# Kernel optimization log

Measured on AMD Instinct MI355X. Metric: run time of the kernel, lower is better.

## Reference

```python
import jax, jax.numpy as jnp
import numpy as np

BN_EPS = 1e-5
L2_EPS = 1e-12


def setup_inputs() -> dict:
    key = jax.random.key(0)
    ks = jax.random.split(key, 4)
    B, C, H, W = 16, 384, 56, 56
    x = jax.random.normal(ks[0], (B, C, H, W), dtype=jnp.float32)
    w_qkv = jax.random.normal(ks[1], (3 * C, C), dtype=jnp.float32) * (1.0 / np.sqrt(C))
    b_qkv = jnp.zeros((3 * C,), dtype=jnp.float32)
    w_proj = jax.random.normal(ks[2], (C, C), dtype=jnp.float32) * (1.0 / np.sqrt(C))
    b_proj = jnp.zeros((C,), dtype=jnp.float32)
    bn_gamma = jnp.ones((C,), dtype=jnp.float32)
    bn_beta = jnp.zeros((C,), dtype=jnp.float32)
    bn_mean = jnp.zeros((C,), dtype=jnp.float32)
    bn_var = jnp.ones((C,), dtype=jnp.float32)
    temperature = jnp.ones((1,), dtype=jnp.float32)
    return {"x": x, "w_qkv": w_qkv, "b_qkv": b_qkv, "w_proj": w_proj,
            "b_proj": b_proj, "bn_gamma": bn_gamma, "bn_beta": bn_beta,
            "bn_mean": bn_mean, "bn_var": bn_var, "temperature": temperature}


def _l2norm_lastdim(t):
    # F.normalize(t, dim=-1): divide by max(||t||_2, eps)
    n = jnp.sqrt(jnp.sum(t * t, axis=-1, keepdims=True))
    return t / jnp.maximum(n, L2_EPS)


def reference(x, w_qkv, b_qkv, w_proj, b_proj, bn_gamma, bn_beta, bn_mean, bn_var, temperature):
    B, C, H, W = x.shape
    N = H * W
    # BatchNorm2d (eval mode, running stats)
    scale = bn_gamma / jnp.sqrt(bn_var + BN_EPS)          # [C]
    shift = bn_beta - bn_mean * scale                     # [C]
    xn = x * scale[None, :, None, None] + shift[None, :, None, None]
    # 1x1 conv qkv: C -> 3C, operate on flattened spatial [B, C, N]
    xn_f = xn.reshape(B, C, N)
    qkv = jnp.einsum('oc,bcn->bon', w_qkv, xn_f) + b_qkv[None, :, None]  # [B,3C,N]
    q, k, v = qkv[:, :C], qkv[:, C:2 * C], qkv[:, 2 * C:]
    q = _l2norm_lastdim(q)                                # [B,C,N]
    k = _l2norm_lastdim(k)
    # channel-transposed attention: [B,C,C]
    logits = jnp.einsum('bcn,bdn->bcd', q, k) * temperature[0]
    attn = jax.nn.softmax(logits, axis=-1)
    fused = jnp.einsum('bcd,bdn->bcn', attn, v)           # [B,C,N]
    # 1x1 proj conv + residual
    out = jnp.einsum('oc,bcn->bon', w_proj, fused) + b_proj[None, :, None]
    return x + out.reshape(B, C, H, W)
```

## Files before the change

kernel.cpp:

```cpp
#include <hip/hip_runtime.h>

#define BATCH 16
#define CCH   384
#define NSP   3136
#define NSPP  3200

typedef unsigned short u16;
typedef float  f32x4  __attribute__((ext_vector_type(4)));
typedef __bf16 bf16x8 __attribute__((ext_vector_type(8)));

__device__ __forceinline__ float bf2f(u16 u) {
  union { unsigned int i; float f; } v; v.i = ((unsigned int)u) << 16; return v.f;
}
__device__ __forceinline__ u16 f2bf(float f) {
  union { float f; unsigned int i; } v; v.f = f;
  unsigned int i = v.i;
  return (u16)((i + 0x7fffu + ((i >> 16) & 1u)) >> 16);
}
__device__ __forceinline__ float rdf(const void* p, long i, bool bf) {
  return bf ? bf2f(((const u16*)p)[i]) : ((const float*)p)[i];
}

__device__ __forceinline__ void gload_lds16(const u16* g, u16* l) {
  __builtin_amdgcn_global_load_lds(
      (const __attribute__((address_space(1))) void*)g,
      (__attribute__((address_space(3))) void*)l, 16, 0, 0);
}

__global__ void transpose_kernel(const void* __restrict__ x, u16* __restrict__ xt,
                                 u16* __restrict__ xbf, const u16* __restrict__ probe) {
  const bool bf = (probe[0] == 0x3F80u);
  __shared__ float Ls[32 * 65];
  const int t = threadIdx.x;
  const int n0 = blockIdx.x * 64, c0 = blockIdx.y * 32, b = blockIdx.z;
  if (n0 >= NSP) {
    const int n_l = t >> 2, c8 = (t & 3) * 8;
    uint4 zq = make_uint4(0, 0, 0, 0);
    *(uint4*)(xt + ((long)b * NSPP + n0 + n_l) * CCH + c0 + c8) = zq;
    return;
  }
  {
    const int c_l = t >> 3, n8 = (t & 7) * 8;
    const long src = ((long)b * CCH + c0 + c_l) * NSP + n0 + n8;
    float v[8];
    if (bf) {
      union { uint4 q; u16 e[8]; } u; u.q = *(const uint4*)((const u16*)x + src);
      #pragma unroll
      for (int i = 0; i < 8; i++) v[i] = bf2f(u.e[i]);
    } else {
      float4 a = *(const float4*)((const float*)x + src);
      float4 c = *(const float4*)((const float*)x + src + 4);
      v[0]=a.x; v[1]=a.y; v[2]=a.z; v[3]=a.w; v[4]=c.x; v[5]=c.y; v[6]=c.z; v[7]=c.w;
    }
    union { uint4 q; u16 e[8]; } ob;
    #pragma unroll
    for (int i = 0; i < 8; i++) { ob.e[i] = f2bf(v[i]); Ls[c_l * 65 + n8 + i] = v[i]; }
    *(uint4*)(xbf + src) = ob.q;
  }
  __syncthreads();
  {
    const int n_l = t >> 2, c8 = (t & 3) * 8;
    union { uint4 q; u16 e[8]; } o;
    #pragma unroll
    for (int i = 0; i < 8; i++) o.e[i] = f2bf(Ls[(c8 + i) * 65 + n_l]);
    *(uint4*)(xt + ((long)b * NSPP + n0 + n_l) * CCH + c0 + c8) = o.q;
  }
}

__global__ void prep_kernel(const void* __restrict__ w_qkv, const void* __restrict__ b_qkv,
                            const void* __restrict__ gamma, const void* __restrict__ beta,
                            const void* __restrict__ mean,  const void* __restrict__ var,
                            const void* __restrict__ b_proj, const void* __restrict__ w_proj,
                            u16* __restrict__ w_eff, float* __restrict__ b_eff,
                            float* __restrict__ bproj_f,
                            unsigned* __restrict__ w2qk, unsigned* __restrict__ wp2,
                            u16* __restrict__ wvT, float* __restrict__ szero,
                            const u16* __restrict__ probe) {
  const bool bf = (probe[0] == 0x3F80u);
  __shared__ float s_scale[CCH], s_shift[CCH];
  const int tid = threadIdx.x;
  const int o = blockIdx.x;
  if (o < 72) {
    szero[o * 256 + tid] = 0.f;
    szero[o * 256 + 128 + tid] = 0.f;
  }
  for (int c = tid; c < CCH; c += 128) {
    float g = rdf(gamma, c, bf), bt = rdf(beta, c, bf);
    float mn = rdf(mean, c, bf), vr = rdf(var, c, bf);
    float sc = g * rsqrtf(vr + 1e-5f);
    s_scale[c] = sc; s_shift[c] = bt - mn * sc;
  }
  __syncthreads();
  float part = 0.f;
  for (int c = tid; c < CCH; c += 128) {
    float w = rdf(w_qkv, (long)o * CCH + c, bf);
    u16 wv = f2bf(w * s_scale[c]);
    w_eff[(long)o * CCH + c] = wv;
    if (o < 768) w2qk[(long)o * CCH + c] = (unsigned)wv | ((unsigned)wv << 16);
    else         wvT[(long)c * CCH + (o - 768)] = wv;
    part += w * s_shift[c];
  }
  for (int off = 32; off > 0; off >>= 1) part += __shfl_down(part, off, 64);
  __shared__ float s_part[2];
  if ((tid & 63) == 0) s_part[tid >> 6] = part;
  __syncthreads();
  if (tid == 0) b_eff[o] = rdf(b_qkv, o, bf) + s_part[0] + s_part[1];
  if (o < CCH) {
    for (int c = tid; c < CCH; c += 128) {
      u16 pv = f2bf(rdf(w_proj, (long)o * CCH + c, bf));
      wp2[(long)o * CCH + c] = (unsigned)pv | ((unsigned)pv << 16);
    }
  }
  if (o == 0) {
    for (int c = tid; c < CCH; c += 128) bproj_f[c] = rdf(b_proj, c, bf);
  }
}

template<int BM, int BN, int WGM, int WGN, int OUTM, bool BIASM, bool RES,
         int NCHK, bool EPIL, bool SUMX, bool SYMM>
__launch_bounds__(256)
__global__ void gemm_nt(const u16* __restrict__ A, const u16* __restrict__ B,
                        void* __restrict__ Cv,
                        const float* __restrict__ biasm,
                        const void* __restrict__ resv,
                        int K, int lda, int ldb, int ldc,
                        long sA, long sB, long sC, long sRes,
                        int zb, int nLim, int ks, int sBM,
                        float* __restrict__ qns, const u16* __restrict__ epW,
                        float* __restrict__ sxp,
                        const u16* __restrict__ probe) {
  constexpr int WM = BM / WGM, WN = BN / WGN;
  constexpr int FM = WM / 16,  FN = WN / 16;
  constexpr int NA = BM / 32,  NB = BN / 32;
  constexpr bool BOUNCE = (OUTM == 1 || OUTM == 2) && (BM == BN) && (WGM == 2) && (WGN == 2);
  const bool f32io = (probe[0] != 0x3F80u);
  __shared__ __align__(16) u16 As[BM * 64];
  __shared__ __align__(16) u16 Bs[BN * 64];
  const int tid = threadIdx.x, wave = tid >> 6, lane = tid & 63;
  const int quad = lane >> 4, l16 = lane & 15;
  const int wm = wave / WGN, wn = wave % WGN;
  int z = blockIdx.z, kc = 0;
  if (ks > 1) { kc = z % ks; z /= ks; }
  A += z * sA; B += z * sB;
  const long cOff = (long)(zb + z) * sC;
  const long rOff = (long)(zb + z) * sRes;

  const int gx = gridDim.x;
  const int tot = gx * gridDim.y;
  const int wg = blockIdx.y * gx + blockIdx.x;
  const int qq = tot >> 3, rr = tot & 7;
  const int xcd = wg & 7, idx = wg >> 3;
  const int nid = (xcd < rr ? xcd * (qq + 1) : rr * (qq + 1) + (xcd - rr) * qq) + idx;
  const int m0 = (nid % gx) * BM, n0 = (nid / gx) * BN;
  if (SYMM && n0 > m0) return;

  const int kLen = K / ks, kBeg = kc * kLen;

  const u16* ag[NA];
  const u16* bg[NB];
  #pragma unroll
  for (int p = 0; p < NA; p++) {
    int u = tid + p * 256, r = u >> 3, k8 = u & 7;
    ag[p] = A + (long)(m0 + r) * lda + kBeg + ((k8 ^ (r & 7)) << 3);
  }
  #pragma unroll
  for (int p = 0; p < NB; p++) {
    int u = tid + p * 256, r = u >> 3, k8 = u & 7;
    bg[p] = B + (long)(n0 + r) * ldb + kBeg + ((k8 ^ (r & 7)) << 3);
  }

  f32x4 acc[FM][FN] = {};
  float rs[FM] = {};

  const int nt = kLen >> 6;
  for (int t = 0; t < nt; t++) {
    #pragma unroll
    for (int p = 0; p < NA; p++) { gload_lds16(ag[p], &As[(p * 256 + wave * 64) * 8]); ag[p] += 64; }
    #pragma unroll
    for (int p = 0; p < NB; p++) { gload_lds16(bg[p], &Bs[(p * 256 + wave * 64) * 8]); bg[p] += 64; }
    __syncthreads();

    #pragma unroll
    for (int tt = 0; tt < 2; tt++) {
      bf16x8 af[FM], bfr[FN];
      #pragma unroll
      for (int f = 0; f < FM; f++) {
        int r = wm * WM + f * 16 + l16;
        af[f] = *(const bf16x8*)&As[r * 64 + (((tt * 4 + quad) ^ (l16 & 7)) << 3)];
      }
      #pragma unroll
      for (int g = 0; g < FN; g++) {
        int r = wn * WN + g * 16 + l16;
        bfr[g] = *(const bf16x8*)&Bs[r * 64 + (((tt * 4 + quad) ^ (l16 & 7)) << 3)];
      }
      if (SUMX) {
        if (n0 == 0 && wn == 0) {
          #pragma unroll
          for (int f = 0; f < FM; f++)
            #pragma unroll
            for (int j = 0; j < 8; j++) rs[f] += (float)af[f][j];
        }
      }
      #pragma unroll
      for (int f = 0; f < FM; f++)
        #pragma unroll
        for (int g = 0; g < FN; g++)
          acc[f][g] = __builtin_amdgcn_mfma_f32_16x16x32_bf16(af[f], bfr[g], acc[f][g], 0, 0, 0);
    }
    __syncthreads();
  }

  if (SUMX) {
    if (n0 == 0 && wn == 0) {
      #pragma unroll
      for (int f = 0; f < FM; f++) {
        float r = rs[f];
        r += __shfl_xor(r, 16, 64);
        r += __shfl_xor(r, 32, 64);
        if (quad == 0) atomicAdd(sxp + (long)z * CCH + m0 + wm * WM + f * 16 + l16, r);
      }
    }
  }

  if (BOUNCE) {
    float* Lb = (float*)As;
    const long cBase = cOff + ((OUTM == 1 && ks > 1) ? (long)kc * sRes : 0L);
    #pragma unroll
    for (int f = 0; f < FM; f++) {
      #pragma unroll
      for (int g = 0; g < FN; g++)
        #pragma unroll
        for (int reg = 0; reg < 4; reg++) {
          float v = acc[f][g][reg];
          if (BIASM) v += biasm[(long)(zb + z) * sBM + m0 + wm * WM + f * 16 + quad * 4 + reg];
          Lb[(wm * 16 + quad * 4 + reg) * BN + wn * WN + g * 16 + l16] = v;
        }
      __syncthreads();
      {
        const int tr = tid >> 3;
        const int cb = (tid & 7) * (BN / 8);
        const int mm = m0 + (tr >> 4) * WM + f * 16 + (tr & 15);
        const long rowBase = (long)mm * ldc;
        #pragma unroll
        for (int j = 0; j < BN / 32; j++) {
          const int nn = n0 + cb + j * 4;
          const bool live = (NCHK != 2) || (nn < nLim);
          if (live) {
            float4 v = *(const float4*)&Lb[tr * BN + cb + j * 4];
            if (RES) {
              if (f32io) {
                float4 r = *(const float4*)&((const float*)resv)[rOff + rowBase + nn];
                v.x += r.x; v.y += r.y; v.z += r.z; v.w += r.w;
              } else {
                const u16* rp = (const u16*)resv + rOff + rowBase + nn;
                v.x += bf2f(rp[0]); v.y += bf2f(rp[1]); v.z += bf2f(rp[2]); v.w += bf2f(rp[3]);
              }
            }
            if (OUTM == 1 || f32io) {
              *(float4*)&((float*)Cv)[cBase + rowBase + nn] = v;
            } else {
              ushort4 o4 = { f2bf(v.x), f2bf(v.y), f2bf(v.z), f2bf(v.w) };
              *(ushort4*)((u16*)Cv + cOff + rowBase + nn) = o4;
            }
          }
        }
      }
      __syncthreads();
    }
  } else {
    #pragma unroll
    for (int f = 0; f < FM; f++) {
      #pragma unroll
      for (int reg = 0; reg < 4; reg++) {
        const int mm = m0 + wm * WM + f * 16 + quad * 4 + reg;
        float s2 = 0.f;
        #pragma unroll
        for (int g = 0; g < FN; g++) {
          int nn = n0 + wn * WN + g * 16 + l16;
          float v = acc[f][g][reg];
          if (BIASM) v += biasm[(long)(zb + z) * sBM + mm];
          long off = (long)mm * ldc + nn;
          bool live = true;
          if (NCHK == 2) live = (nn < nLim);
          if (NCHK == 3) live = (mm < nLim);
          if (RES && live) {
            long ro = rOff + off;
            v += f32io ? ((const float*)resv)[ro] : bf2f(((const u16*)resv)[ro]);
          }
          if (EPIL) s2 += v * bf2f(epW[(long)mm * CCH + nn]);
          if (OUTM == 1) {
            ((float*)Cv)[cOff + off + (long)kc * sRes] = v;
          } else if (OUTM == 2) {
            if (live) {
              if (f32io) ((float*)Cv)[cOff + off] = v;
              else       ((u16*)Cv)[cOff + off]   = f2bf(v);
            }
          } else if (OUTM == 4) {
            if (live) {
              u16 hi = f2bf(v);
              u16 lo = f2bf(v - bf2f(hi));
              ((unsigned*)Cv)[cOff + off] = (unsigned)hi | ((unsigned)lo << 16);
            }
          } else {
            if (live) ((u16*)Cv)[cOff + off] = f2bf(v);
          }
        }
        if (EPIL) {
          s2 += __shfl_xor(s2, 1, 16);
          s2 += __shfl_xor(s2, 2, 16);
          s2 += __shfl_xor(s2, 4, 16);
          s2 += __shfl_xor(s2, 8, 16);
          if (l16 == 0) atomicAdd(qns + (long)(zb + z) * 768 + mm, s2);
        }
      }
    }
  }
}

__global__ void gred_ugemv_kernel(const float* __restrict__ Gp, unsigned* __restrict__ Gs,
                                  const u16* __restrict__ w_eff, const float* __restrict__ sx,
                                  float* __restrict__ u, int kspl) {
  const int b = blockIdx.y, bx = blockIdx.x, tid = threadIdx.x;
  if (bx < 576) {
    const int idx = bx * 256 + tid;
    const int r = idx / CCH, c = idx % CCH;
    const long e = ((r >> 7) >= (c >> 7)) ? ((long)r * CCH + c) : ((long)c * CCH + r);
    const long base = (long)b * kspl * (CCH * CCH);
    float s = 0.f;
    for (int k = 0; k < kspl; k++) s += Gp[base + (long)k * (CCH * CCH) + e];
    u16 hi = f2bf(s);
    u16 lo = f2bf(s - bf2f(hi));
    Gs[(long)b * (CCH * CCH) + idx] = (unsigned)hi | ((unsigned)lo << 16);
  } else {
    const int m = (bx - 576) * 4 + (tid >> 6), l = tid & 63;
    float s = 0.f;
    for (int k = l; k < CCH; k += 64) s += bf2f(w_eff[(long)m * CCH + k]) * sx[b * CCH + k];
    for (int off = 32; off > 0; off >>= 1) s += __shfl_down(s, off, 64);
    if (l == 0) u[b * 768 + m] = s;
  }
}

__global__ void cgemv_kernel(const unsigned* __restrict__ wp2, const float* __restrict__ av,
                             const float* __restrict__ bproj, float* __restrict__ cvec) {
  const int o = blockIdx.x, b = blockIdx.y, l = threadIdx.x;
  float s = 0.f;
  for (int c = l; c < CCH; c += 64)
    s += bf2f((u16)(wp2[(long)o * CCH + c] & 0xffffu)) * av[b * CCH + c];
  for (int off = 32; off > 0; off >>= 1) s += __shfl_down(s, off, 64);
  if (l == 0) cvec[b * CCH + o] = s + bproj[o];
}

__global__ void softmax_kernel(const float* __restrict__ Lg, const float* __restrict__ qn2,
                               const float* __restrict__ u, const float* __restrict__ beff,
                               const void* __restrict__ temp,
                               u16* __restrict__ attn, float* __restrict__ av,
                               const u16* __restrict__ probe) {
  const bool bfm = (probe[0] == 0x3F80u);
  const int c = blockIdx.x, b = blockIdx.y, tid = threadIdx.x;
  const float* row = Lg + ((long)b * CCH + c) * CCH;
  const float beq = beff[c], uq = u[b * 768 + c];
  const float qn = qn2[b * 768 + c] + 2.f * beq * uq + 3136.f * beq * beq;
  const float rq = 1.f / fmaxf(sqrtf(fmaxf(qn, 0.f)), 1e-12f);
  const float T = rdf(temp, 0, bfm);
  float v[3]; float mx = -1e30f;
  #pragma unroll
  for (int j = 0; j < 3; j++) {
    int d = tid + j * 128;
    float bek = beff[384 + d], uk = u[b * 768 + 384 + d];
    float kn = qn2[b * 768 + 384 + d] + 2.f * bek * uk + 3136.f * bek * bek;
    float rd = 1.f / fmaxf(sqrtf(fmaxf(kn, 0.f)), 1e-12f);
    float lg = row[d] + uq * bek + beq * uk + 3136.f * beq * bek;
    v[j] = lg * rq * rd * T;
    mx = fmaxf(mx, v[j]);
  }
  for (int off = 32; off > 0; off >>= 1) mx = fmaxf(mx, __shfl_down(mx, off, 64));
  __shared__ float sm[2];
  if ((tid & 63) == 0) sm[tid >> 6] = mx;
  __syncthreads();
  mx = fmaxf(sm[0], sm[1]);
  float s = 0.f;
  #pragma unroll
  for (int j = 0; j < 3; j++) { v[j] = __expf(v[j] - mx); s += v[j]; }
  for (int off = 32; off > 0; off >>= 1) s += __shfl_down(s, off, 64);
  __shared__ float ss[2];
  if ((tid & 63) == 0) ss[tid >> 6] = s;
  __syncthreads();
  s = ss[0] + ss[1];
  const float inv = 1.f / s;
  float avp = 0.f;
  u16* arow = attn + ((long)b * CCH + c) * CCH;
  #pragma unroll
  for (int j = 0; j < 3; j++) {
    float p = v[j] * inv;
    arow[tid + j * 128] = f2bf(p);
    avp += p * beff[768 + tid + j * 128];
  }
  for (int off = 32; off > 0; off >>= 1) avp += __shfl_down(avp, off, 64);
  __shared__ float sa[2];
  if ((tid & 63) == 0) sa[tid >> 6] = avp;
  __syncthreads();
  if (tid == 0) av[b * CCH + c] = sa[0] + sa[1];
}

extern "C" void kernel_launch(void* const* d_in, const int* in_sizes, int n_in,
                              void* d_out, int out_size, void* d_ws, size_t ws_size,
                              hipStream_t stream) {
  const void* x      = d_in[0];
  const void* w_qkv  = d_in[1];
  const void* b_qkv  = d_in[2];
  const void* w_proj = d_in[3];
  const void* b_proj = d_in[4];
  const void* gamma  = d_in[5];
  const void* beta   = d_in[6];
  const void* mean   = d_in[7];
  const void* var    = d_in[8];
  const void* temp   = d_in[9];
  const u16* probe = (const u16*)gamma;

  const size_t SZ_XT   = (size_t)BATCH * NSPP * CCH * 2;
  const size_t SZ_XBF  = (size_t)BATCH * CCH * NSP * 2;
  const size_t SZ_WEFF = (size_t)1152 * CCH * 2;
  const size_t SZ_W2QK = (size_t)768 * CCH * 4;
  const size_t SZ_WP2  = (size_t)CCH * CCH * 4;
  const size_t SZ_WVT  = (size_t)CCH * CCH * 2;
  const size_t SZ_BEFF = (size_t)1152 * 4;
  const size_t SZ_BPRJ = (size_t)CCH * 4;
  const size_t SZ_U    = (size_t)BATCH * 768 * 4;
  const size_t SZ_AV   = (size_t)BATCH * CCH * 4;
  const size_t SZ_CV   = (size_t)BATCH * CCH * 4;
  const size_t SZ_MM   = (size_t)BATCH * CCH * CCH;
  const size_t FIXED = SZ_XT + SZ_XBF + SZ_WEFF + SZ_W2QK + SZ_WP2 + SZ_WVT +
                       SZ_BEFF + SZ_BPRJ + (size_t)BATCH * (CCH + 768) * 4 +
                       SZ_U + SZ_AV + SZ_CV +
                       SZ_MM * 4  + SZ_MM * 4  + SZ_MM * 4  +
                       SZ_MM * 2  + SZ_MM * 4  + SZ_MM * 2 ;
  int kspl = 7;
  if (ws_size < FIXED + (size_t)BATCH * 7 * CCH * CCH * 4) kspl = 1;

  char* ws = (char*)d_ws;
  u16*      xt    = (u16*)ws;      ws += SZ_XT;
  u16*      xbf   = (u16*)ws;      ws += SZ_XBF;
  u16*      w_eff = (u16*)ws;      ws += SZ_WEFF;
  unsigned* w2qk  = (unsigned*)ws; ws += SZ_W2QK;
  unsigned* wp2   = (unsigned*)ws; ws += SZ_WP2;
  u16*      wvT   = (u16*)ws;      ws += SZ_WVT;
  float*    b_eff = (float*)ws;    ws += SZ_BEFF;
  float*    bproj = (float*)ws;    ws += SZ_BPRJ;
  float*    sx    = (float*)ws;    ws += (size_t)BATCH * CCH * 4;
  float*    qn2   = (float*)ws;    ws += (size_t)BATCH * 768 * 4;
  float*    u     = (float*)ws;    ws += SZ_U;
  float*    av    = (float*)ws;    ws += SZ_AV;
  float*    cvec  = (float*)ws;    ws += SZ_CV;
  unsigned* Gs    = (unsigned*)ws; ws += SZ_MM * 4;
  unsigned* Ts    = (unsigned*)ws; ws += SZ_MM * 4;
  float*    Lg    = (float*)ws;    ws += SZ_MM * 4;
  u16*      attn  = (u16*)ws;      ws += SZ_MM * 2;
  unsigned* RTs   = (unsigned*)ws; ws += SZ_MM * 4;
  u16*      Mb    = (u16*)ws;      ws += SZ_MM * 2;
  float*    Gp    = (float*)ws;

  const long sXB = (long)CCH * NSP;
  const long sMM = (long)CCH * CCH;
  const long sM2 = (long)CCH * 768;

  transpose_kernel<<<dim3(NSPP / 64, CCH / 32, BATCH), dim3(256), 0, stream>>>(
      x, xt, xbf, probe);
  prep_kernel<<<dim3(1152), dim3(128), 0, stream>>>(
      w_qkv, b_qkv, gamma, beta, mean, var, b_proj, w_proj,
      w_eff, b_eff, bproj, w2qk, wp2, wvT, sx, probe);

  gemm_nt<128, 128, 2, 2, 1, false, false, 0, false, true, true>
      <<<dim3(3, 3, BATCH * kspl), dim3(256), 0, stream>>>(
      xbf, xbf, Gp, nullptr, nullptr,
      NSP, NSP, NSP, CCH, sXB, sXB, (long)kspl * sMM, sMM,
      0, 0, kspl, 0, nullptr, nullptr, sx, probe);

  gred_ugemv_kernel<<<dim3(768, BATCH), dim3(256), 0, stream>>>(
      Gp, Gs, w_eff, sx, u, kspl);

  gemm_nt<96, 96, 2, 2, 4, false, false, 3, true, false, false>
      <<<dim3(8, 4, BATCH), dim3(256), 0, stream>>>(
      (const u16*)w2qk, (const u16*)Gs, Ts, nullptr, nullptr,
      768, 768, 768, CCH, 0L, sM2, sMM, 0L,
      0, CCH, 1, 0, qn2, w_eff, nullptr, probe);

  gemm_nt<96, 96, 2, 2, 1, false, false, 0, false, false, false>
      <<<dim3(4, 4, BATCH), dim3(256), 0, stream>>>(
      (const u16*)Ts, (const u16*)w2qk + (long)384 * 768, Lg, nullptr, nullptr,
      768, 768, 768, CCH, sM2, 0L, sMM, 0L,
      0, 0, 1, 0, nullptr, nullptr, nullptr, probe);

  softmax_kernel<<<dim3(CCH, BATCH), dim3(128), 0, stream>>>(
      Lg, qn2, u, b_eff, temp, attn, av, probe);

  gemm_nt<96, 96, 2, 2, 4, false, false, 0, false, false, false>
      <<<dim3(4, 4, BATCH), dim3(256), 0, stream>>>(
      wvT, attn, RTs, nullptr, nullptr,
      CCH, CCH, CCH, CCH, 0L, sMM, sMM, 0L,
      0, 0, 1, 0, nullptr, nullptr, nullptr, probe);

  cgemv_kernel<<<dim3(CCH, BATCH), dim3(64), 0, stream>>>(wp2, av, bproj, cvec);

  gemm_nt<96, 96, 2, 2, 0, false, false, 0, false, false, false>
      <<<dim3(4, 4, BATCH), dim3(256), 0, stream>>>(
      (const u16*)wp2, (const u16*)RTs, Mb, nullptr, nullptr,
      768, 768, 768, CCH, 0L, sM2, sMM, 0L,
      0, 0, 1, 0, nullptr, nullptr, nullptr, probe);

  gemm_nt<128, 128, 2, 2, 2, true, true, 2, false, false, false>
      <<<dim3(3, 25, BATCH), dim3(256), 0, stream>>>(
      Mb, xt, d_out, cvec, x,
      CCH, CCH, CCH, NSP, sMM, (long)NSPP * CCH, (long)CCH * NSP, (long)CCH * NSP,
      0, NSP, 1, CCH, nullptr, nullptr, nullptr, probe);
}
```

Baseline: 378.0 us.

## Drop split-K Gram GEMM and write packed output directly with mirror pass

The X·Xᵀ Gram GEMM no longer splits K into 7 chunks that write fp32 partials to a large workspace buffer. Each block now runs the full K=3136 loop and writes the packed hi/lo bf16 result straight into Gs. A lighter kernel then copies the computed lower-triangle tiles into the missing upper-triangle tiles, alongside the existing u GEMV. This removes the write and reduction of the per-batch partial Gram buffers, at the cost of far fewer blocks (96 active) each running a long serial K loop. The LDS bounce buffer is also padded by 4 floats per row to reduce bank conflicts.

```diff
diff --git a/kernel.cpp b/kernel.cpp
--- a/kernel.cpp
+++ b/kernel.cpp
@@ -125,22 +125,27 @@
                         const void* __restrict__ resv,
                         int K, int lda, int ldb, int ldc,
                         long sA, long sB, long sC, long sRes,
-                        int zb, int nLim, int ks, int sBM,
+                        int zb, int nLim, int sBM,
                         float* __restrict__ qns, const u16* __restrict__ epW,
                         float* __restrict__ sxp,
                         const u16* __restrict__ probe) {
   constexpr int WM = BM / WGM, WN = BN / WGN;
   constexpr int FM = WM / 16,  FN = WN / 16;
   constexpr int NA = BM / 32,  NB = BN / 32;
-  constexpr bool BOUNCE = (OUTM == 1 || OUTM == 2) && (BM == BN) && (WGM == 2) && (WGN == 2);
+  constexpr bool BOUNCE = (OUTM == 1 || OUTM == 2) && (BM == BN) && (WGN == 2);
+  constexpr int RPF = WGM * 16;
+  constexpr int LBS = BN + 4;
+  constexpr int SM_STAGE  = (BM + BN) * 128;
+  constexpr int SM_BOUNCE = BOUNCE ? RPF * LBS * 4 : 0;
+  constexpr int SM_BYTES  = SM_STAGE > SM_BOUNCE ? SM_STAGE : SM_BOUNCE;
+  __shared__ __align__(16) char smem[SM_BYTES];
+  u16* As = (u16*)smem;
+  u16* Bs = (u16*)(smem + BM * 128);
   const bool f32io = (probe[0] != 0x3F80u);
-  __shared__ __align__(16) u16 As[BM * 64];
-  __shared__ __align__(16) u16 Bs[BN * 64];
   const int tid = threadIdx.x, wave = tid >> 6, lane = tid & 63;
   const int quad = lane >> 4, l16 = lane & 15;
   const int wm = wave / WGN, wn = wave % WGN;
-  int z = blockIdx.z, kc = 0;
-  if (ks > 1) { kc = z % ks; z /= ks; }
+  const int z = blockIdx.z;
   A += z * sA; B += z * sB;
   const long cOff = (long)(zb + z) * sC;
   const long rOff = (long)(zb + z) * sRes;
@@ -154,25 +159,23 @@
   const int m0 = (nid % gx) * BM, n0 = (nid / gx) * BN;
   if (SYMM && n0 > m0) return;
 
-  const int kLen = K / ks, kBeg = kc * kLen;
-
   const u16* ag[NA];
   const u16* bg[NB];
   #pragma unroll
   for (int p = 0; p < NA; p++) {
     int u = tid + p * 256, r = u >> 3, k8 = u & 7;
-    ag[p] = A + (long)(m0 + r) * lda + kBeg + ((k8 ^ (r & 7)) << 3);
+    ag[p] = A + (long)(m0 + r) * lda + ((k8 ^ (r & 7)) << 3);
   }
   #pragma unroll
   for (int p = 0; p < NB; p++) {
     int u = tid + p * 256, r = u >> 3, k8 = u & 7;
-    bg[p] = B + (long)(n0 + r) * ldb + kBeg + ((k8 ^ (r & 7)) << 3);
+    bg[p] = B + (long)(n0 + r) * ldb + ((k8 ^ (r & 7)) << 3);
   }
 
   f32x4 acc[FM][FN] = {};
   float rs[FM] = {};
 
-  const int nt = kLen >> 6;
+  const int nt = K >> 6;
   for (int t = 0; t < nt; t++) {
     #pragma unroll
     for (int p = 0; p < NA; p++) { gload_lds16(ag[p], &As[(p * 256 + wave * 64) * 8]); ag[p] += 64; }
@@ -223,8 +226,7 @@
   }
 
   if (BOUNCE) {
-    float* Lb = (float*)As;
-    const long cBase = cOff + ((OUTM == 1 && ks > 1) ? (long)kc * sRes : 0L);
+    float* Lb = (float*)smem;
     #pragma unroll
     for (int f = 0; f < FM; f++) {
       #pragma unroll
@@ -233,7 +235,7 @@
         for (int reg = 0; reg < 4; reg++) {
           float v = acc[f][g][reg];
           if (BIASM) v += biasm[(long)(zb + z) * sBM + m0 + wm * WM + f * 16 + quad * 4 + reg];
-          Lb[(wm * 16 + quad * 4 + reg) * BN + wn * WN + g * 16 + l16] = v;
+          Lb[(wm * 16 + quad * 4 + reg) * LBS + wn * WN + g * 16 + l16] = v;
         }
       __syncthreads();
       {
@@ -246,7 +248,7 @@
           const int nn = n0 + cb + j * 4;
           const bool live = (NCHK != 2) || (nn < nLim);
           if (live) {
-            float4 v = *(const float4*)&Lb[tr * BN + cb + j * 4];
+            float4 v = *(const float4*)&Lb[tr * LBS + cb + j * 4];
             if (RES) {
               if (f32io) {
                 float4 r = *(const float4*)&((const float*)resv)[rOff + rowBase + nn];
@@ -257,7 +259,7 @@
               }
             }
             if (OUTM == 1 || f32io) {
-              *(float4*)&((float*)Cv)[cBase + rowBase + nn] = v;
+              *(float4*)&((float*)Cv)[cOff + rowBase + nn] = v;
             } else {
               ushort4 o4 = { f2bf(v.x), f2bf(v.y), f2bf(v.z), f2bf(v.w) };
               *(ushort4*)((u16*)Cv + cOff + rowBase + nn) = o4;
@@ -289,7 +291,7 @@
           }
           if (EPIL) s2 += v * bf2f(epW[(long)mm * CCH + nn]);
           if (OUTM == 1) {
-            ((float*)Cv)[cOff + off + (long)kc * sRes] = v;
+            ((float*)Cv)[cOff + off] = v;
           } else if (OUTM == 2) {
             if (live) {
               if (f32io) ((float*)Cv)[cOff + off] = v;
@@ -317,22 +319,21 @@
   }
 }
 
-__global__ void gred_ugemv_kernel(const float* __restrict__ Gp, unsigned* __restrict__ Gs,
-                                  const u16* __restrict__ w_eff, const float* __restrict__ sx,
-                                  float* __restrict__ u, int kspl) {
+__global__ void mirror_ugemv_kernel(unsigned* __restrict__ Gs,
+                                    const u16* __restrict__ w_eff,
+                                    const float* __restrict__ sx,
+                                    float* __restrict__ u) {
   const int b = blockIdx.y, bx = blockIdx.x, tid = threadIdx.x;
-  if (bx < 576) {
-    const int idx = bx * 256 + tid;
-    const int r = idx / CCH, c = idx % CCH;
-    const long e = ((r >> 7) >= (c >> 7)) ? ((long)r * CCH + c) : ((long)c * CCH + r);
-    const long base = (long)b * kspl * (CCH * CCH);
-    float s = 0.f;
-    for (int k = 0; k < kspl; k++) s += Gp[base + (long)k * (CCH * CCH) + e];
-    u16 hi = f2bf(s);
-    u16 lo = f2bf(s - bf2f(hi));
-    Gs[(long)b * (CCH * CCH) + idx] = (unsigned)hi | ((unsigned)lo << 16);
+  if (bx < 192) {
+    const int q = bx >> 6;
+    const int e = (bx & 63) * 256 + tid;
+    const int r = e >> 7, c = e & 127;
+    const int r0 = (q == 2) ? 128 : 0;
+    const int c0 = (q == 0) ? 128 : 256;
+    const long base = (long)b * (CCH * CCH);
+    Gs[base + (long)(r0 + r) * CCH + (c0 + c)] = Gs[base + (long)(c0 + c) * CCH + (r0 + r)];
   } else {
-    const int m = (bx - 576) * 4 + (tid >> 6), l = tid & 63;
+    const int m = (bx - 192) * 4 + (tid >> 6), l = tid & 63;
     float s = 0.f;
     for (int k = l; k < CCH; k += 64) s += bf2f(w_eff[(long)m * CCH + k]) * sx[b * CCH + k];
     for (int off = 32; off > 0; off >>= 1) s += __shfl_down(s, off, 64);
@@ -429,13 +430,6 @@
   const size_t SZ_AV   = (size_t)BATCH * CCH * 4;
   const size_t SZ_CV   = (size_t)BATCH * CCH * 4;
   const size_t SZ_MM   = (size_t)BATCH * CCH * CCH;
-  const size_t FIXED = SZ_XT + SZ_XBF + SZ_WEFF + SZ_W2QK + SZ_WP2 + SZ_WVT +
-                       SZ_BEFF + SZ_BPRJ + (size_t)BATCH * (CCH + 768) * 4 +
-                       SZ_U + SZ_AV + SZ_CV +
-                       SZ_MM * 4  + SZ_MM * 4  + SZ_MM * 4  +
-                       SZ_MM * 2  + SZ_MM * 4  + SZ_MM * 2 ;
-  int kspl = 7;
-  if (ws_size < FIXED + (size_t)BATCH * 7 * CCH * CCH * 4) kspl = 1;
 
   char* ws = (char*)d_ws;
   u16*      xt    = (u16*)ws;      ws += SZ_XT;
@@ -457,7 +451,6 @@
   u16*      attn  = (u16*)ws;      ws += SZ_MM * 2;
   unsigned* RTs   = (unsigned*)ws; ws += SZ_MM * 4;
   u16*      Mb    = (u16*)ws;      ws += SZ_MM * 2;
-  float*    Gp    = (float*)ws;
 
   const long sXB = (long)CCH * NSP;
   const long sMM = (long)CCH * CCH;
@@ -469,26 +462,26 @@
       w_qkv, b_qkv, gamma, beta, mean, var, b_proj, w_proj,
       w_eff, b_eff, bproj, w2qk, wp2, wvT, sx, probe);
 
-  gemm_nt<128, 128, 2, 2, 1, false, false, 0, false, true, true>
-      <<<dim3(3, 3, BATCH * kspl), dim3(256), 0, stream>>>(
-      xbf, xbf, Gp, nullptr, nullptr,
-      NSP, NSP, NSP, CCH, sXB, sXB, (long)kspl * sMM, sMM,
-      0, 0, kspl, 0, nullptr, nullptr, sx, probe);
-
-  gred_ugemv_kernel<<<dim3(768, BATCH), dim3(256), 0, stream>>>(
-      Gp, Gs, w_eff, sx, u, kspl);
+  gemm_nt<128, 128, 2, 2, 4, false, false, 0, false, true, true>
+      <<<dim3(3, 3, BATCH), dim3(256), 0, stream>>>(
+      xbf, xbf, Gs, nullptr, nullptr,
+      NSP, NSP, NSP, CCH, sXB, sXB, sMM, 0L,
+      0, 0, 0, nullptr, nullptr, sx, probe);
+
+  mirror_ugemv_kernel<<<dim3(384, BATCH), dim3(256), 0, stream>>>(
+      Gs, w_eff, sx, u);
 
   gemm_nt<96, 96, 2, 2, 4, false, false, 3, true, false, false>
       <<<dim3(8, 4, BATCH), dim3(256), 0, stream>>>(
       (const u16*)w2qk, (const u16*)Gs, Ts, nullptr, nullptr,
       768, 768, 768, CCH, 0L, sM2, sMM, 0L,
-      0, CCH, 1, 0, qn2, w_eff, nullptr, probe);
+      0, CCH, 0, qn2, w_eff, nullptr, probe);
 
   gemm_nt<96, 96, 2, 2, 1, false, false, 0, false, false, false>
       <<<dim3(4, 4, BATCH), dim3(256), 0, stream>>>(
       (const u16*)Ts, (const u16*)w2qk + (long)384 * 768, Lg, nullptr, nullptr,
       768, 768, 768, CCH, sM2, 0L, sMM, 0L,
-      0, 0, 1, 0, nullptr, nullptr, nullptr, probe);
+      0, 0, 0, nullptr, nullptr, nullptr, probe);
 
   softmax_kernel<<<dim3(CCH, BATCH), dim3(128), 0, stream>>>(
       Lg, qn2, u, b_eff, temp, attn, av, probe);
@@ -497,7 +490,7 @@
       <<<dim3(4, 4, BATCH), dim3(256), 0, stream>>>(
       wvT, attn, RTs, nullptr, nullptr,
       CCH, CCH, CCH, CCH, 0L, sMM, sMM, 0L,
-      0, 0, 1, 0, nullptr, nullptr, nullptr, probe);
+      0, 0, 0, nullptr, nullptr, nullptr, probe);
 
   cgemv_kernel<<<dim3(CCH, BATCH), dim3(64), 0, stream>>>(wp2, av, bproj, cvec);
 
@@ -505,11 +498,11 @@
       <<<dim3(4, 4, BATCH), dim3(256), 0, stream>>>(
       (const u16*)wp2, (const u16*)RTs, Mb, nullptr, nullptr,
       768, 768, 768, CCH, 0L, sM2, sMM, 0L,
-      0, 0, 1, 0, nullptr, nullptr, nullptr, probe);
+      0, 0, 0, nullptr, nullptr, nullptr, probe);
 
   gemm_nt<128, 128, 2, 2, 2, true, true, 2, false, false, false>
       <<<dim3(3, 25, BATCH), dim3(256), 0, stream>>>(
       Mb, xt, d_out, cvec, x,
       CCH, CCH, CCH, NSP, sMM, (long)NSPP * CCH, (long)CCH * NSP, (long)CCH * NSP,
-      0, NSP, 1, CCH, nullptr, nullptr, nullptr, probe);
-}
+      0, NSP, CCH, nullptr, nullptr, nullptr, probe);
+}
```

Result: no change. 376.2 us (-0.5%).
